# Performance work log

Measured on AMD Instinct MI355X. Metric: run time of the kernel, lower is better.

## Reference

```python
import jax, jax.numpy as jnp
import numpy as np

N_NODES = 50000
N_EDGES = 600000
N_GRAPHS = 64
D = 128  # node/edge/global feature dim
NUM_CLASSES = 10
NUM_PASSES = 3


def setup_inputs() -> dict:
    key = jax.random.key(0)
    ks = jax.random.split(key, 12)
    node_attr = jax.random.normal(ks[0], (N_NODES, D), jnp.float32)
    edge_attr = jax.random.normal(ks[1], (N_EDGES, D), jnp.float32)
    u = jax.random.normal(ks[2], (N_GRAPHS, D), jnp.float32)
    edge_index = jax.random.randint(ks[3], (2, N_EDGES), 0, N_NODES, jnp.int64 if jax.config.jax_enable_x64 else jnp.int32)
    batch = jnp.sort(jax.random.randint(ks[4], (N_NODES,), 0, N_GRAPHS, jnp.int32))
    s = 1.0 / np.sqrt(D)
    We_w = jax.random.normal(ks[5], (4 * D, D), jnp.float32) * s
    We_b = jnp.zeros((D,), jnp.float32)
    Wn_w = jax.random.normal(ks[6], (3 * D, D), jnp.float32) * s
    Wn_b = jnp.zeros((D,), jnp.float32)
    Wg_w = jax.random.normal(ks[7], (3 * D, D), jnp.float32) * s
    Wg_b = jnp.zeros((D,), jnp.float32)
    lin_w = jax.random.normal(ks[8], (3 * D, NUM_CLASSES), jnp.float32) * s
    lin_b = jnp.zeros((NUM_CLASSES,), jnp.float32)
    return {"node_attr": node_attr, "edge_attr": edge_attr, "u": u,
            "edge_index": edge_index, "batch": batch,
            "We_w": We_w, "We_b": We_b, "Wn_w": Wn_w, "Wn_b": Wn_b,
            "Wg_w": Wg_w, "Wg_b": Wg_b, "lin_w": lin_w, "lin_b": lin_b}


def _segment_mean(x, seg, num_segments):
    s = jax.ops.segment_sum(x, seg, num_segments=num_segments)
    cnt = jax.ops.segment_sum(jnp.ones((x.shape[0],), x.dtype), seg, num_segments=num_segments)
    return s / jnp.maximum(cnt, 1.0)[:, None]


def reference(node_attr, edge_attr, u, edge_index, batch,
              We_w, We_b, Wn_w, Wn_b, Wg_w, Wg_b, lin_w, lin_b):
    src = edge_index[0]
    dst = edge_index[1]
    n_nodes = node_attr.shape[0]
    n_graphs = u.shape[0]
    edge_bar = None
    for _ in range(NUM_PASSES):
        # edge update: phi_e([h_src, h_dst, e, u[batch_src]])
        e_in = jnp.concatenate(
            [node_attr[src], node_attr[dst], edge_attr, u[batch[src]]], axis=1)
        edge_attr = jax.nn.relu(e_in @ We_w + We_b)
        # node update: mean of incoming edges per dest node, then phi_n
        edge_bar = _segment_mean(edge_attr, dst, n_nodes)  # [N, D]
        n_in = jnp.concatenate([node_attr, edge_bar, u[batch]], axis=1)
        node_attr = jax.nn.relu(n_in @ Wn_w + Wn_b)
        # global update: per-graph means, then phi_g
        node_mean = _segment_mean(node_attr, batch, n_graphs)
        eb_mean = _segment_mean(edge_bar, batch, n_graphs)
        g_in = jnp.concatenate([node_mean, eb_mean, u], axis=1)
        u = jax.nn.relu(g_in @ Wg_w + Wg_b)
    # readout: concat + global mean pool + linear classifier
    graph_attr = jnp.concatenate([node_attr, edge_bar, u[batch]], axis=1)  # [N, 3D]
    pooled = _segment_mean(graph_attr, batch, n_graphs)  # [G, 3D]
    return pooled @ lin_w + lin_b
```

## Files before the change

### kernel.cpp

```cpp
#include <hip/hip_runtime.h>
#include <math.h>

#define D 128

typedef short bf16x8 __attribute__((ext_vector_type(8)));
typedef float f32x4 __attribute__((ext_vector_type(4)));
typedef ushort ushort8 __attribute__((ext_vector_type(8)));

__device__ __forceinline__ ushort f2b(float f) {
    union { float f; unsigned u; } v; v.f = f;
    unsigned r = v.u + 0x7FFFu + ((v.u >> 16) & 1u);
    return (ushort)(r >> 16);
}
__device__ __forceinline__ float b2f(ushort b) {
    union { unsigned u; float f; } v; v.u = ((unsigned)b) << 16;
    return v.f;
}
__device__ __forceinline__ void gl_lds16(const void* g, void* l) {
    __builtin_amdgcn_global_load_lds(
        (const __attribute__((address_space(1))) void*)g,
        (__attribute__((address_space(3))) void*)l, 16, 0, 0);
}
__device__ __forceinline__ int lower_bound_i(const int* __restrict__ a, int n, int v) {
    int lo = 0, hi = n;
    while (lo < hi) { int m = (lo + hi) >> 1; if (a[m] < v) lo = m + 1; else hi = m; }
    return lo;
}

__global__ void count_kernel(const int* __restrict__ dst, int* __restrict__ cnt, int E) {
    int e = blockIdx.x * blockDim.x + threadIdx.x;
    if (e < E) atomicAdd(&cnt[dst[e]], 1);
}

__global__ void scan_kernel(const int* __restrict__ cnt, int* __restrict__ offs, int N) {
    __shared__ int part[1024];
    const int t = threadIdx.x;
    const int chunk = (N + 1023) >> 10;
    int lo = t * chunk; if (lo > N) lo = N;
    int hi = lo + chunk; if (hi > N) hi = N;
    int s = 0;
    for (int i = lo; i < hi; ++i) s += cnt[i];
    part[t] = s;
    __syncthreads();
    if (t == 0) {
        int a = 0;
        for (int i = 0; i < 1024; ++i) { int v = part[i]; part[i] = a; a += v; }
        offs[N] = a;
    }
    __syncthreads();
    int a = part[t];
    for (int i = lo; i < hi; ++i) { offs[i] = a; a += cnt[i]; }
}

__global__ void scatter_kernel(const int* __restrict__ dst, const int* __restrict__ offs,
                               int* __restrict__ fill, int* __restrict__ csr, int E) {
    int e = blockIdx.x * blockDim.x + threadIdx.x;
    if (e < E) {
        int d = dst[e];
        int p = offs[d] + atomicAdd(&fill[d], 1);
        csr[p] = e;
    }
}

__global__ void prep_kernel(
    float* __restrict__ edge,
    const float* __restrict__ node, ushort* __restrict__ node_bf,
    const float* __restrict__ u, ushort* __restrict__ u_bf,
    const float* __restrict__ We_w, ushort* __restrict__ Bt12, ushort* __restrict__ W3t,
    const float* __restrict__ Wn_w, ushort* __restrict__ Wnt,
    int N, int G, int E)
{
    const int gid = blockIdx.x * 256 + threadIdx.x;
    const int c0 = E * 32;
    const int c1 = c0 + N * D / 4;
    const int c2 = c1 + G * D / 4;
    const int c3 = c2 + 512 * D;
    const int c4 = c3 + 384 * D;
    if (gid < c0) {
        int row = gid >> 5, q = gid & 31;
        float4 v = *(const float4*)(edge + (size_t)row * D + q * 4);
        ushort4 o; o.x = f2b(v.x); o.y = f2b(v.y); o.z = f2b(v.z); o.w = f2b(v.w);
        *(ushort4*)((ushort*)edge + (size_t)row * 256 + q * 4) = o;
    } else if (gid < c1) {
        int i = (gid - c0) * 4;
        float4 v = *(const float4*)(node + i);
        ushort4 o; o.x = f2b(v.x); o.y = f2b(v.y); o.z = f2b(v.z); o.w = f2b(v.w);
        *(ushort4*)(node_bf + i) = o;
    } else if (gid < c2) {
        int i = (gid - c1) * 4;
        float4 v = *(const float4*)(u + i);
        ushort4 o; o.x = f2b(v.x); o.y = f2b(v.y); o.z = f2b(v.z); o.w = f2b(v.w);
        *(ushort4*)(u_bf + i) = o;
    } else if (gid < c3) {
        int i = gid - c2;
        int k = i >> 7, n = i & 127;
        if (k < 384) {
            ushort b = f2b(We_w[i]);
            if (k < 256)
                Bt12[(((size_t)((k >> 7) << 7) + n) << 7) + (k & 127)] = b;
            else
                W3t[((size_t)n << 7) + (k - 256)] = b;
        }
    } else if (gid < c4) {
        int i = gid - c3;
        int k = i >> 7, n = i & 127;
        Wnt[(size_t)n * 384 + k] = f2b(Wn_w[i]);
    }
}

__global__ void uproj_kernel(const float* __restrict__ u, const float* __restrict__ We_w,
                             const float* __restrict__ We_b, float* __restrict__ upf)
{
    __shared__ float us[128];
    const int g = blockIdx.x;
    const int j = threadIdx.x;
    us[j] = u[g * D + j];
    __syncthreads();
    float s = We_b[j];
    for (int k = 0; k < 128; ++k) s += us[k] * We_w[(size_t)(384 + k) * D + j];
    upf[g * D + j] = s;
}

__global__ __launch_bounds__(256) void nproj_gemm(
    const ushort* __restrict__ node_bf, const ushort* __restrict__ Bt12,
    const float* __restrict__ upf, const int* __restrict__ batch,
    float* __restrict__ npf, int N)
{
    __shared__ ushort As[128 * 32];
    __shared__ ushort Bs[256 * 32];
    __shared__ int rbs[128];

    const int tid = threadIdx.x;
    const int w = tid >> 6, l = tid & 63;
    const int n0 = blockIdx.x * 128;

    if (tid < 128) {
        int n = n0 + tid; if (n >= N) n = N - 1;
        rbs[tid] = batch[n];
    }

    f32x4 acc[4][8];
#pragma unroll
    for (int i = 0; i < 4; ++i)
#pragma unroll
        for (int j = 0; j < 8; ++j) acc[i][j] = (f32x4)0.0f;

    const int wm = (w >> 1) * 64, wn = (w & 1) * 128;
    const int srow = l >> 2;
    const int part = (l & 3) * 8;

    for (int c = 0; c < 4; ++c) {
        const int kl = c * 32;
#pragma unroll
        for (int t = 0; t < 2; ++t) {
            const int s = w + t * 4;
            int n = n0 + s * 16 + srow; if (n >= N) n = N - 1;
            gl_lds16(node_bf + (size_t)n * D + kl + part, &As[s * 512]);
        }
#pragma unroll
        for (int t = 0; t < 4; ++t) {
            const int s = w * 4 + t;
            const int br = s * 16 + srow;
            const int h = br >> 7, b7 = br & 127;
            const int n = (h << 7) | ((b7 & 15) << 3) | (b7 >> 4);
            gl_lds16(Bt12 + (size_t)n * 128 + kl + part, &Bs[s * 512]);
        }
        __syncthreads();

        bf16x8 af[4], bfr[8];
#pragma unroll
        for (int i = 0; i < 4; ++i)
            af[i] = *(const bf16x8*)&As[(wm + i * 16 + (l & 15)) * 32 + (l >> 4) * 8];
#pragma unroll
        for (int j = 0; j < 8; ++j)
            bfr[j] = *(const bf16x8*)&Bs[(wn + j * 16 + (l & 15)) * 32 + (l >> 4) * 8];
#pragma unroll
        for (int i = 0; i < 4; ++i)
#pragma unroll
            for (int j = 0; j < 8; ++j)
                acc[i][j] = __builtin_amdgcn_mfma_f32_16x16x32_bf16(af[i], bfr[j], acc[i][j], 0, 0, 0);
        __syncthreads();
    }

    const int cc = l & 15;
    const int qr = (l >> 4) * 4;
#pragma unroll
    for (int i = 0; i < 4; ++i) {
#pragma unroll
        for (int r = 0; r < 4; ++r) {
            const int m = wm + i * 16 + qr + r;
            const int n = n0 + m;
            if (n < N) {
                float4 u0 = make_float4(0.f, 0.f, 0.f, 0.f);
                float4 u1 = make_float4(0.f, 0.f, 0.f, 0.f);
                if (wn == 0) {
                    const float* pu = upf + (size_t)rbs[m] * D + cc * 8;
                    u0 = *(const float4*)pu;
                    u1 = *(const float4*)(pu + 4);
                }
                float4 o0, o1;
                o0.x = acc[i][0][r] + u0.x; o0.y = acc[i][1][r] + u0.y;
                o0.z = acc[i][2][r] + u0.z; o0.w = acc[i][3][r] + u0.w;
                o1.x = acc[i][4][r] + u1.x; o1.y = acc[i][5][r] + u1.y;
                o1.z = acc[i][6][r] + u1.z; o1.w = acc[i][7][r] + u1.w;
                float* op = npf + (size_t)n * 256 + wn + cc * 8;
                *(float4*)op = o0;
                *(float4*)(op + 4) = o1;
            }
        }
    }
}

__global__ __launch_bounds__(256, 2) void edge_gemm(
    ushort* __restrict__ edge_u,
    const float* __restrict__ npf,
    const int* __restrict__ src, const int* __restrict__ dst,
    const ushort* __restrict__ W3t, int E)
{
    __shared__ ushort As[256 * 32];
    __shared__ ushort Bs[128 * 32];
    __shared__ int rs[256], rd[256];

    const int tid = threadIdx.x;
    const int w = tid >> 6, l = tid & 63;
    const int e0 = blockIdx.x * 256;

    {
        int e = e0 + tid; if (e >= E) e = E - 1;
        rs[tid] = src[e]; rd[tid] = dst[e];
    }

    f32x4 acc[4][8];
#pragma unroll
    for (int i = 0; i < 4; ++i)
#pragma unroll
        for (int j = 0; j < 8; ++j) acc[i][j] = (f32x4)0.0f;

    const int wm = w * 64;
    const int srow = l >> 2;
    const int part = (l & 3) * 8;

    __syncthreads();

    for (int c = 0; c < 4; ++c) {
        const int kl = c * 32;

#pragma unroll
        for (int t = 0; t < 4; ++t) {
            const int s = w * 4 + t;
            int e = e0 + s * 16 + srow; if (e >= E) e = E - 1;
            gl_lds16(edge_u + (size_t)e * 256 + kl + part, &As[s * 512]);
        }
#pragma unroll
        for (int t = 0; t < 2; ++t) {
            const int s = w + t * 4;
            const int br = s * 16 + srow;
            const int n = ((br & 15) << 3) | (br >> 4);
            gl_lds16(W3t + (size_t)n * 128 + kl + part, &Bs[s * 512]);
        }
        __syncthreads();

        bf16x8 af[4], bfr[8];
#pragma unroll
        for (int i = 0; i < 4; ++i)
            af[i] = *(const bf16x8*)&As[(wm + i * 16 + (l & 15)) * 32 + (l >> 4) * 8];
#pragma unroll
        for (int j = 0; j < 8; ++j)
            bfr[j] = *(const bf16x8*)&Bs[(j * 16 + (l & 15)) * 32 + (l >> 4) * 8];
#pragma unroll
        for (int i = 0; i < 4; ++i)
#pragma unroll
            for (int j = 0; j < 8; ++j)
                acc[i][j] = __builtin_amdgcn_mfma_f32_16x16x32_bf16(af[i], bfr[j], acc[i][j], 0, 0, 0);
        __syncthreads();
    }

    const int cc = l & 15;
    const int qr = (l >> 4) * 4;
#pragma unroll
    for (int i = 0; i < 4; ++i) {
#pragma unroll
        for (int r = 0; r < 4; ++r) {
            const int m = wm + i * 16 + qr + r;
            const int e = e0 + m;
            if (e < E) {
                const float* p1 = npf + (size_t)rs[m] * 256 + cc * 8;
                const float* p2 = npf + (size_t)rd[m] * 256 + 128 + cc * 8;
                float4 a0 = *(const float4*)p1;
                float4 a1 = *(const float4*)(p1 + 4);
                float4 b0 = *(const float4*)p2;
                float4 b1 = *(const float4*)(p2 + 4);
                ushort8 o;
                o[0] = f2b(fmaxf(acc[i][0][r] + a0.x + b0.x, 0.0f));
                o[1] = f2b(fmaxf(acc[i][1][r] + a0.y + b0.y, 0.0f));
                o[2] = f2b(fmaxf(acc[i][2][r] + a0.z + b0.z, 0.0f));
                o[3] = f2b(fmaxf(acc[i][3][r] + a0.w + b0.w, 0.0f));
                o[4] = f2b(fmaxf(acc[i][4][r] + a1.x + b1.x, 0.0f));
                o[5] = f2b(fmaxf(acc[i][5][r] + a1.y + b1.y, 0.0f));
                o[6] = f2b(fmaxf(acc[i][6][r] + a1.z + b1.z, 0.0f));
                o[7] = f2b(fmaxf(acc[i][7][r] + a1.w + b1.w, 0.0f));
                *(ushort8*)(edge_u + (size_t)e * 256 + cc * 8) = o;
            }
        }
    }
}

__global__ void gather_ebar(const ushort* __restrict__ edge_u, const int* __restrict__ offs,
                            const int* __restrict__ csr, ushort* __restrict__ ebar_bf, int N)
{
    int n = blockIdx.x * 8 + (threadIdx.x >> 5);
    int q = threadIdx.x & 31;
    if (n >= N) return;
    int lo = offs[n], hi = offs[n + 1];
    float s0 = 0.0f, s1 = 0.0f, s2 = 0.0f, s3 = 0.0f;
    for (int j = lo; j < hi; ++j) {
        int e = csr[j];
        ushort4 v = *(const ushort4*)(edge_u + (size_t)e * 256 + q * 4);
        s0 += b2f(v.x); s1 += b2f(v.y); s2 += b2f(v.z); s3 += b2f(v.w);
    }
    float inv = 1.0f / (float)max(hi - lo, 1);
    ushort4 o; o.x = f2b(s0 * inv); o.y = f2b(s1 * inv); o.z = f2b(s2 * inv); o.w = f2b(s3 * inv);
    *(ushort4*)(ebar_bf + (size_t)n * D + q * 4) = o;
}

__global__ __launch_bounds__(256) void node_gemm(
    ushort* __restrict__ node_bf, const ushort* __restrict__ ebar_bf,
    const ushort* __restrict__ u_bf, const int* __restrict__ batch,
    const ushort* __restrict__ Wt, const float* __restrict__ bias, int N)
{
    __shared__ ushort As[128 * 32];
    __shared__ ushort Bs[128 * 32];
    __shared__ int rb[128];

    const int tid = threadIdx.x;
    const int w = tid >> 6, l = tid & 63;
    const int n0 = blockIdx.x * 128;

    if (tid < 128) {
        int n = n0 + tid; if (n >= N) n = N - 1;
        rb[tid] = batch[n];
    }

    f32x4 acc[4][4];
#pragma unroll
    for (int i = 0; i < 4; ++i)
#pragma unroll
        for (int j = 0; j < 4; ++j) acc[i][j] = (f32x4)0.0f;

    const int wm = (w >> 1) * 64, wn = (w & 1) * 64;
    float bj4[4];
#pragma unroll
    for (int j = 0; j < 4; ++j) bj4[j] = bias[wn + j * 16 + (l & 15)];

    const int srow = l >> 2;
    const int part = (l & 3) * 8;

    __syncthreads();

    for (int c = 0; c < 12; ++c) {
        const int srcsel = c >> 2;
        const int kl = (c & 3) * 32;

#pragma unroll
        for (int t = 0; t < 2; ++t) {
            const int s = w + t * 4;
            const int row = s * 16 + srow;
            int n = n0 + row; if (n >= N) n = N - 1;
            const ushort* gp;
            if (srcsel == 0)      gp = node_bf + (size_t)n * D + kl + part;
            else if (srcsel == 1) gp = ebar_bf + (size_t)n * D + kl + part;
            else                  gp = u_bf + (size_t)rb[row] * D + kl + part;
            gl_lds16(gp, &As[s * 512]);
        }
#pragma unroll
        for (int t = 0; t < 2; ++t) {
            const int s = w + t * 4;
            const int n = s * 16 + srow;
            gl_lds16(Wt + (size_t)n * 384 + c * 32 + part, &Bs[s * 512]);
        }
        __syncthreads();

        bf16x8 af[4], bfr[4];
#pragma unroll
        for (int i = 0; i < 4; ++i)
            af[i] = *(const bf16x8*)&As[(wm + i * 16 + (l & 15)) * 32 + (l >> 4) * 8];
#pragma unroll
        for (int j = 0; j < 4; ++j)
            bfr[j] = *(const bf16x8*)&Bs[(wn + j * 16 + (l & 15)) * 32 + (l >> 4) * 8];
#pragma unroll
        for (int i = 0; i < 4; ++i)
#pragma unroll
            for (int j = 0; j < 4; ++j)
                acc[i][j] = __builtin_amdgcn_mfma_f32_16x16x32_bf16(af[i], bfr[j], acc[i][j], 0, 0, 0);
        __syncthreads();
    }

#pragma unroll
    for (int i = 0; i < 4; ++i) {
#pragma unroll
        for (int r = 0; r < 4; ++r) {
            const int m = wm + i * 16 + (l >> 4) * 4 + r;
            const int n = n0 + m;
            if (n < N) {
#pragma unroll
                for (int j = 0; j < 4; ++j) {
                    float v = fmaxf(acc[i][j][r] + bj4[j], 0.0f);
                    node_bf[(size_t)n * D + wn + j * 16 + (l & 15)] = f2b(v);
                }
            }
        }
    }
}

__global__ void reduce_partial(
    const ushort* __restrict__ node_bf, const ushort* __restrict__ ebar_bf,
    const int* __restrict__ batch,
    float* __restrict__ nsum, float* __restrict__ esum, int N)
{
    const int col = threadIdx.x & 127;
    const int half = threadIdx.x >> 7;
    const int r0 = blockIdx.x * 128;
    float sn = 0.0f, se = 0.0f;
    int cur = -1;
    for (int ri = half; ri < 128; ri += 2) {
        int r = r0 + ri;
        if (r >= N) break;
        int g = batch[r];
        if (g != cur) {
            if (cur >= 0) {
                atomicAdd(&nsum[cur * D + col], sn);
                atomicAdd(&esum[cur * D + col], se);
            }
            cur = g; sn = 0.0f; se = 0.0f;
        }
        sn += b2f(node_bf[(size_t)r * D + col]);
        se += b2f(ebar_bf[(size_t)r * D + col]);
    }
    if (cur >= 0) {
        atomicAdd(&nsum[cur * D + col], sn);
        atomicAdd(&esum[cur * D + col], se);
    }
}

__global__ void finalize_global(
    float* __restrict__ nsum, float* __restrict__ esum,
    const int* __restrict__ batch,
    float* __restrict__ nmean, float* __restrict__ emean,
    float* __restrict__ u, ushort* __restrict__ u_bf,
    const float* __restrict__ W, const float* __restrict__ bias, int N)
{
    __shared__ float gin[384];
    __shared__ int cnt_s;
    const int g = blockIdx.x;
    const int j = threadIdx.x;
    if (j == 0) {
        int lo = lower_bound_i(batch, N, g);
        int hi = lower_bound_i(batch, N, g + 1);
        cnt_s = hi - lo;
    }
    __syncthreads();
    float inv = 1.0f / (float)max(cnt_s, 1);
    float nm = nsum[g * D + j] * inv;
    float em = esum[g * D + j] * inv;
    nmean[g * D + j] = nm;
    emean[g * D + j] = em;
    nsum[g * D + j] = 0.0f;
    esum[g * D + j] = 0.0f;
    gin[j] = nm; gin[128 + j] = em; gin[256 + j] = u[g * D + j];
    __syncthreads();
    float s = bias[j];
    for (int k = 0; k < 384; ++k) s += gin[k] * W[(size_t)k * D + j];
    float v = fmaxf(s, 0.0f);
    u[g * D + j] = v;
    u_bf[g * D + j] = f2b(v);
}

__global__ void out_kernel(
    const float* __restrict__ nmean, const float* __restrict__ emean,
    const float* __restrict__ u, const int* __restrict__ batch,
    const float* __restrict__ lw, const float* __restrict__ lb,
    float* __restrict__ out, int N, int NC)
{
    __shared__ float pin[384];
    __shared__ int cntg;
    const int g = blockIdx.x;
    const int t = threadIdx.x;
    if (t == 0) {
        int lo = lower_bound_i(batch, N, g);
        int hi = lower_bound_i(batch, N, g + 1);
        cntg = hi - lo;
    }
    __syncthreads();
    if (t < 128)       pin[t] = nmean[g * D + t];
    else if (t < 256)  pin[t] = emean[g * D + (t - 128)];
    else               pin[t] = (cntg > 0) ? u[g * D + (t - 256)] : 0.0f;
    __syncthreads();
    int c = t >> 5, wv = t & 31;
    if (c < NC) {
        float s = 0.0f;
        for (int k = wv; k < 384; k += 32) s += pin[k] * lw[(size_t)k * NC + c];
#pragma unroll
        for (int off = 16; off > 0; off >>= 1) s += __shfl_down(s, off, 32);
        if (wv == 0) out[g * NC + c] = s + lb[c];
    }
}

extern "C" void kernel_launch(void* const* d_in, const int* in_sizes, int n_in,
                              void* d_out, int out_size, void* d_ws, size_t ws_size,
                              hipStream_t stream) {
    float* node = (float*)d_in[0];
    float* edge = (float*)d_in[1];
    float* u    = (float*)d_in[2];
    const int* eidx  = (const int*)d_in[3];
    const int* batch = (const int*)d_in[4];
    const float* We_w = (const float*)d_in[5];
    const float* We_b = (const float*)d_in[6];
    const float* Wn_w = (const float*)d_in[7];
    const float* Wn_b = (const float*)d_in[8];
    const float* Wg_w = (const float*)d_in[9];
    const float* Wg_b = (const float*)d_in[10];
    const float* lin_w = (const float*)d_in[11];
    const float* lin_b = (const float*)d_in[12];

    const int N = in_sizes[0] / D;
    const int E = in_sizes[3] / 2;
    const int G = in_sizes[2] / D;
    const int NC = out_size / G;
    const int* src = eidx;
    const int* dst = eidx + E;

    char* p = (char*)d_ws;
    auto carve = [&](size_t bytes) { void* r = p; p += (bytes + 255) & ~(size_t)255; return r; };
    int*    cnt     = (int*)carve((size_t)N * 4);
    int*    fill    = (int*)carve((size_t)N * 4);
    float*  nsum    = (float*)carve((size_t)G * D * 4);
    float*  esum    = (float*)carve((size_t)G * D * 4);
    size_t  zspan   = (size_t)(p - (char*)cnt);
    int*    offs    = (int*)carve((size_t)(N + 1) * 4);
    int*    csr     = (int*)carve((size_t)E * 4);
    ushort* node_bf = (ushort*)carve((size_t)N * D * 2);
    ushort* ebar_bf = (ushort*)carve((size_t)N * D * 2);
    ushort* u_bf    = (ushort*)carve((size_t)G * D * 2);
    ushort* Bt12    = (ushort*)carve((size_t)256 * 128 * 2);
    ushort* W3t     = (ushort*)carve((size_t)128 * 128 * 2);
    ushort* Wnt     = (ushort*)carve((size_t)384 * D * 2);
    float*  nmean   = (float*)carve((size_t)G * D * 4);
    float*  emean   = (float*)carve((size_t)G * D * 4);
    float*  upf     = (float*)carve((size_t)G * D * 4);
    float*  npf     = (float*)carve((size_t)N * 256 * 4);

    ushort* edge_u = (ushort*)edge;

    hipMemsetAsync(cnt, 0, zspan, stream);

    count_kernel<<<(E + 255) / 256, 256, 0, stream>>>(dst, cnt, E);
    scan_kernel<<<1, 1024, 0, stream>>>(cnt, offs, N);
    scatter_kernel<<<(E + 255) / 256, 256, 0, stream>>>(dst, offs, fill, csr, E);

    const int prep_units = E * 32 + N * D / 4 + G * D / 4 + 512 * D + 384 * D;
    prep_kernel<<<(prep_units + 255) / 256, 256, 0, stream>>>(
        edge, node, node_bf, u, u_bf, We_w, Bt12, W3t, Wn_w, Wnt, N, G, E);

    const int edge_blocks = (E + 255) / 256;
    const int node_blocks = (N + 127) / 128;
    const int proj_blocks = (N + 127) / 128;
    const int red_blocks  = (N + 127) / 128;

    for (int pass = 0; pass < 3; ++pass) {
        uproj_kernel<<<G, 128, 0, stream>>>(u, We_w, We_b, upf);
        nproj_gemm<<<proj_blocks, 256, 0, stream>>>(node_bf, Bt12, upf, batch, npf, N);
        edge_gemm<<<edge_blocks, 256, 0, stream>>>(edge_u, npf, src, dst, W3t, E);
        gather_ebar<<<(N + 7) / 8, 256, 0, stream>>>(edge_u, offs, csr, ebar_bf, N);
        node_gemm<<<node_blocks, 256, 0, stream>>>(node_bf, ebar_bf, u_bf, batch,
                                                   Wnt, Wn_b, N);
        reduce_partial<<<red_blocks, 256, 0, stream>>>(node_bf, ebar_bf, batch, nsum, esum, N);
        finalize_global<<<G, 128, 0, stream>>>(nsum, esum, batch, nmean, emean,
                                               u, u_bf, Wg_w, Wg_b, N);
    }
    out_kernel<<<G, 384, 0, stream>>>(nmean, emean, u, batch, lin_w, lin_b,
                                      (float*)d_out, N, NC);
}
```

Baseline: 1.329 ms.

## Process edges in dst-sorted CSR order and store node projections partly in bf16

Edges are permuted into destination-sorted order, with src/dst ids stored per sorted slot. The edge GEMM then writes its output contiguously in that order into the upper half of each row of the edge buffer, and the first pass reads the original edges through the CSR indirection. This lets gather_ebar read contiguous rows without the csr lookup and gives better locality for the dst projection loads. The src-side node projection is also stored in bf16 to halve its gather traffic, at some loss of precision. The scheme depends on the input edge buffer being reused as a ping-pong region whose halves are addressed as rows 2e and 2e+1.

```diff
diff --git a/kernel.cpp b/kernel.cpp
--- a/kernel.cpp
+++ b/kernel.cpp
@@ -52,13 +52,17 @@
     for (int i = lo; i < hi; ++i) { offs[i] = a; a += cnt[i]; }
 }
 
-__global__ void scatter_kernel(const int* __restrict__ dst, const int* __restrict__ offs,
-                               int* __restrict__ fill, int* __restrict__ csr, int E) {
+__global__ void scatter_kernel(const int* __restrict__ dst, const int* __restrict__ src,
+                               const int* __restrict__ offs,
+                               int* __restrict__ fill, int* __restrict__ csr,
+                               int* __restrict__ srcp, int* __restrict__ dstp, int E) {
     int e = blockIdx.x * blockDim.x + threadIdx.x;
     if (e < E) {
         int d = dst[e];
         int p = offs[d] + atomicAdd(&fill[d], 1);
         csr[p] = e;
+        srcp[p] = src[e];
+        dstp[p] = d;
     }
 }
 
@@ -124,7 +128,7 @@
 __global__ __launch_bounds__(256) void nproj_gemm(
     const ushort* __restrict__ node_bf, const ushort* __restrict__ Bt12,
     const float* __restrict__ upf, const int* __restrict__ batch,
-    float* __restrict__ npf, int N)
+    ushort* __restrict__ npb, float* __restrict__ npf2, int N)
 {
     __shared__ ushort As[128 * 32];
     __shared__ ushort Bs[256 * 32];
@@ -191,35 +195,45 @@
             const int m = wm + i * 16 + qr + r;
             const int n = n0 + m;
             if (n < N) {
-                float4 u0 = make_float4(0.f, 0.f, 0.f, 0.f);
-                float4 u1 = make_float4(0.f, 0.f, 0.f, 0.f);
                 if (wn == 0) {
                     const float* pu = upf + (size_t)rbs[m] * D + cc * 8;
-                    u0 = *(const float4*)pu;
-                    u1 = *(const float4*)(pu + 4);
+                    float4 u0 = *(const float4*)pu;
+                    float4 u1 = *(const float4*)(pu + 4);
+                    ushort8 o;
+                    o[0] = f2b(acc[i][0][r] + u0.x);
+                    o[1] = f2b(acc[i][1][r] + u0.y);
+                    o[2] = f2b(acc[i][2][r] + u0.z);
+                    o[3] = f2b(acc[i][3][r] + u0.w);
+                    o[4] = f2b(acc[i][4][r] + u1.x);
+                    o[5] = f2b(acc[i][5][r] + u1.y);
+                    o[6] = f2b(acc[i][6][r] + u1.z);
+                    o[7] = f2b(acc[i][7][r] + u1.w);
+                    *(ushort8*)(npb + (size_t)n * 128 + cc * 8) = o;
+                } else {
+                    float4 o0, o1;
+                    o0.x = acc[i][0][r]; o0.y = acc[i][1][r];
+                    o0.z = acc[i][2][r]; o0.w = acc[i][3][r];
+                    o1.x = acc[i][4][r]; o1.y = acc[i][5][r];
+                    o1.z = acc[i][6][r]; o1.w = acc[i][7][r];
+                    float* op = npf2 + (size_t)n * 128 + cc * 8;
+                    *(float4*)op = o0;
+                    *(float4*)(op + 4) = o1;
                 }
-                float4 o0, o1;
-                o0.x = acc[i][0][r] + u0.x; o0.y = acc[i][1][r] + u0.y;
-                o0.z = acc[i][2][r] + u0.z; o0.w = acc[i][3][r] + u0.w;
-                o1.x = acc[i][4][r] + u1.x; o1.y = acc[i][5][r] + u1.y;
-                o1.z = acc[i][6][r] + u1.z; o1.w = acc[i][7][r] + u1.w;
-                float* op = npf + (size_t)n * 256 + wn + cc * 8;
-                *(float4*)op = o0;
-                *(float4*)(op + 4) = o1;
             }
         }
     }
 }
 
 __global__ __launch_bounds__(256, 2) void edge_gemm(
-    ushort* __restrict__ edge_u,
-    const float* __restrict__ npf,
-    const int* __restrict__ src, const int* __restrict__ dst,
-    const ushort* __restrict__ W3t, int E)
+    ushort* __restrict__ edge_buf,
+    const int* __restrict__ csr,
+    const int* __restrict__ srcp, const int* __restrict__ dstp,
+    const ushort* __restrict__ npb, const float* __restrict__ npf2,
+    const ushort* __restrict__ W3t, int E, int pass0)
 {
     __shared__ ushort As[256 * 32];
     __shared__ ushort Bs[128 * 32];
-    __shared__ int rs[256], rd[256];
+    __shared__ int rs[256], rd[256], rc[256];
 
     const int tid = threadIdx.x;
     const int w = tid >> 6, l = tid & 63;
@@ -227,7 +241,8 @@
 
     {
         int e = e0 + tid; if (e >= E) e = E - 1;
-        rs[tid] = src[e]; rd[tid] = dst[e];
+        rs[tid] = srcp[e]; rd[tid] = dstp[e];
+        rc[tid] = pass0 ? (csr[e] * 2) : (e * 2 + 1);
     }
 
     f32x4 acc[4][8];
@@ -248,8 +263,8 @@
 #pragma unroll
         for (int t = 0; t < 4; ++t) {
             const int s = w * 4 + t;
-            int e = e0 + s * 16 + srow; if (e >= E) e = E - 1;
-            gl_lds16(edge_u + (size_t)e * 256 + kl + part, &As[s * 512]);
+            const int row = s * 16 + srow;
+            gl_lds16(edge_buf + (size_t)rc[row] * 128 + kl + part, &As[s * 512]);
         }
 #pragma unroll
         for (int t = 0; t < 2; ++t) {
@@ -284,29 +299,27 @@
             const int m = wm + i * 16 + qr + r;
             const int e = e0 + m;
             if (e < E) {
-                const float* p1 = npf + (size_t)rs[m] * 256 + cc * 8;
-                const float* p2 = npf + (size_t)rd[m] * 256 + 128 + cc * 8;
-                float4 a0 = *(const float4*)p1;
-                float4 a1 = *(const float4*)(p1 + 4);
+                ushort8 p1 = *(const ushort8*)(npb + (size_t)rs[m] * 128 + cc * 8);
+                const float* p2 = npf2 + (size_t)rd[m] * 128 + cc * 8;
                 float4 b0 = *(const float4*)p2;
                 float4 b1 = *(const float4*)(p2 + 4);
                 ushort8 o;
-                o[0] = f2b(fmaxf(acc[i][0][r] + a0.x + b0.x, 0.0f));
-                o[1] = f2b(fmaxf(acc[i][1][r] + a0.y + b0.y, 0.0f));
-                o[2] = f2b(fmaxf(acc[i][2][r] + a0.z + b0.z, 0.0f));
-                o[3] = f2b(fmaxf(acc[i][3][r] + a0.w + b0.w, 0.0f));
-                o[4] = f2b(fmaxf(acc[i][4][r] + a1.x + b1.x, 0.0f));
-                o[5] = f2b(fmaxf(acc[i][5][r] + a1.y + b1.y, 0.0f));
-                o[6] = f2b(fmaxf(acc[i][6][r] + a1.z + b1.z, 0.0f));
-                o[7] = f2b(fmaxf(acc[i][7][r] + a1.w + b1.w, 0.0f));
-                *(ushort8*)(edge_u + (size_t)e * 256 + cc * 8) = o;
+                o[0] = f2b(fmaxf(acc[i][0][r] + b2f(p1[0]) + b0.x, 0.0f));
+                o[1] = f2b(fmaxf(acc[i][1][r] + b2f(p1[1]) + b0.y, 0.0f));
+                o[2] = f2b(fmaxf(acc[i][2][r] + b2f(p1[2]) + b0.z, 0.0f));
+                o[3] = f2b(fmaxf(acc[i][3][r] + b2f(p1[3]) + b0.w, 0.0f));
+                o[4] = f2b(fmaxf(acc[i][4][r] + b2f(p1[4]) + b1.x, 0.0f));
+                o[5] = f2b(fmaxf(acc[i][5][r] + b2f(p1[5]) + b1.y, 0.0f));
+                o[6] = f2b(fmaxf(acc[i][6][r] + b2f(p1[6]) + b1.z, 0.0f));
+                o[7] = f2b(fmaxf(acc[i][7][r] + b2f(p1[7]) + b1.w, 0.0f));
+                *(ushort8*)(edge_buf + (size_t)e * 256 + 128 + cc * 8) = o;
             }
         }
     }
 }
 
-__global__ void gather_ebar(const ushort* __restrict__ edge_u, const int* __restrict__ offs,
-                            const int* __restrict__ csr, ushort* __restrict__ ebar_bf, int N)
+__global__ void gather_ebar(const ushort* __restrict__ edge_buf, const int* __restrict__ offs,
+                            ushort* __restrict__ ebar_bf, int N)
 {
     int n = blockIdx.x * 8 + (threadIdx.x >> 5);
     int q = threadIdx.x & 31;
@@ -314,8 +327,7 @@
     int lo = offs[n], hi = offs[n + 1];
     float s0 = 0.0f, s1 = 0.0f, s2 = 0.0f, s3 = 0.0f;
     for (int j = lo; j < hi; ++j) {
-        int e = csr[j];
-        ushort4 v = *(const ushort4*)(edge_u + (size_t)e * 256 + q * 4);
+        ushort4 v = *(const ushort4*)(edge_buf + (size_t)j * 256 + 128 + q * 4);
         s0 += b2f(v.x); s1 += b2f(v.y); s2 += b2f(v.z); s3 += b2f(v.w);
     }
     float inv = 1.0f / (float)max(hi - lo, 1);
@@ -538,6 +550,8 @@
     size_t  zspan   = (size_t)(p - (char*)cnt);
     int*    offs    = (int*)carve((size_t)(N + 1) * 4);
     int*    csr     = (int*)carve((size_t)E * 4);
+    int*    srcp    = (int*)carve((size_t)E * 4);
+    int*    dstp    = (int*)carve((size_t)E * 4);
     ushort* node_bf = (ushort*)carve((size_t)N * D * 2);
     ushort* ebar_bf = (ushort*)carve((size_t)N * D * 2);
     ushort* u_bf    = (ushort*)carve((size_t)G * D * 2);
@@ -547,15 +561,17 @@
     float*  nmean   = (float*)carve((size_t)G * D * 4);
     float*  emean   = (float*)carve((size_t)G * D * 4);
     float*  upf     = (float*)carve((size_t)G * D * 4);
-    float*  npf     = (float*)carve((size_t)N * 256 * 4);
-
-    ushort* edge_u = (ushort*)edge;
+    ushort* npb     = (ushort*)carve((size_t)N * 128 * 2);
+    float*  npf2    = (float*)carve((size_t)N * 128 * 4);
+
+    ushort* edge_bf = (ushort*)edge;
 
     hipMemsetAsync(cnt, 0, zspan, stream);
 
     count_kernel<<<(E + 255) / 256, 256, 0, stream>>>(dst, cnt, E);
     scan_kernel<<<1, 1024, 0, stream>>>(cnt, offs, N);
-    scatter_kernel<<<(E + 255) / 256, 256, 0, stream>>>(dst, offs, fill, csr, E);
+    scatter_kernel<<<(E + 255) / 256, 256, 0, stream>>>(dst, src, offs, fill, csr,
+                                                        srcp, dstp, E);
 
     const int prep_units = E * 32 + N * D / 4 + G * D / 4 + 512 * D + 384 * D;
     prep_kernel<<<(prep_units + 255) / 256, 256, 0, stream>>>(
@@ -568,9 +584,11 @@
 
     for (int pass = 0; pass < 3; ++pass) {
         uproj_kernel<<<G, 128, 0, stream>>>(u, We_w, We_b, upf);
-        nproj_gemm<<<proj_blocks, 256, 0, stream>>>(node_bf, Bt12, upf, batch, npf, N);
-        edge_gemm<<<edge_blocks, 256, 0, stream>>>(edge_u, npf, src, dst, W3t, E);
-        gather_ebar<<<(N + 7) / 8, 256, 0, stream>>>(edge_u, offs, csr, ebar_bf, N);
+        nproj_gemm<<<proj_blocks, 256, 0, stream>>>(node_bf, Bt12, upf, batch,
+                                                    npb, npf2, N);
+        edge_gemm<<<edge_blocks, 256, 0, stream>>>(edge_bf, csr, srcp, dstp,
+                                                   npb, npf2, W3t, E, pass == 0 ? 1 : 0);
+        gather_ebar<<<(N + 7) / 8, 256, 0, stream>>>(edge_bf, offs, ebar_bf, N);
         node_gemm<<<node_blocks, 256, 0, stream>>>(node_bf, ebar_bf, u_bf, batch,
                                                    Wnt, Wn_b, N);
         reduce_partial<<<red_blocks, 256, 0, stream>>>(node_bf, ebar_bf, batch, nsum, esum, N);
```

Result: faster. 1.205 ms (-9.3%).
